# Kernel tuning notes

Measured on AMD Instinct MI355X. Metric: run time of the kernel, lower is better.

## Reference

```python
import jax, jax.numpy as jnp
import numpy as np

N = 6000
E = 48000
NODE_TYPE_SIZE = 9
OBSTACLE = 1
RADIUS = 0.03
EPS = 1e-8


def _safe_norm(x):
    # L2 norm over last dim, safe gradient at 0 (diagonal / self edges)
    sq = jnp.sum(x * x, axis=-1, keepdims=True)
    return jnp.where(sq > 0, jnp.sqrt(jnp.where(sq > 0, sq, 1.0)), 0.0)


def setup_inputs() -> dict:
    key = jax.random.key(0)
    ks = jax.random.split(key, 12)
    world_pos = jax.random.uniform(ks[0], (N, 3), dtype=jnp.float32)
    prev_world_pos = world_pos + 0.001 * jax.random.normal(ks[1], (N, 3), dtype=jnp.float32)
    mesh_pos = jax.random.uniform(ks[2], (N, 2), dtype=jnp.float32)
    node_type = jax.random.randint(ks[3], (N, 1), 0, NODE_TYPE_SIZE)
    senders = jax.random.randint(ks[4], (E,), 0, N)
    receivers = jax.random.randint(ks[5], (E,), 0, N)
    node_mean = jax.random.normal(ks[6], (3 + NODE_TYPE_SIZE,), dtype=jnp.float32)
    node_std = 0.5 + jax.random.uniform(ks[7], (3 + NODE_TYPE_SIZE,), dtype=jnp.float32)
    mesh_mean = jax.random.normal(ks[8], (7,), dtype=jnp.float32)
    mesh_std = 0.5 + jax.random.uniform(ks[9], (7,), dtype=jnp.float32)
    world_mean = jax.random.normal(ks[10], (4,), dtype=jnp.float32)
    world_std = 0.5 + jax.random.uniform(ks[11], (4,), dtype=jnp.float32)
    return dict(world_pos=world_pos, prev_world_pos=prev_world_pos, mesh_pos=mesh_pos,
                node_type=node_type, senders=senders, receivers=receivers,
                node_mean=node_mean, node_std=node_std, mesh_mean=mesh_mean,
                mesh_std=mesh_std, world_mean=world_mean, world_std=world_std)


def reference(world_pos, prev_world_pos, mesh_pos, node_type, senders, receivers,
              node_mean, node_std, mesh_mean, mesh_std, world_mean, world_std):
    n = world_pos.shape[0]
    # --- node features: velocity + one-hot node type, normalized ---
    velocity = world_pos - prev_world_pos
    one_hot = jax.nn.one_hot(node_type[:, 0], NODE_TYPE_SIZE, dtype=world_pos.dtype)
    node_feat = jnp.concatenate([velocity, one_hot], axis=-1)  # [N, 12]
    node_out = (node_feat - node_mean) / jnp.maximum(node_std, EPS)
    # --- radius graph: dense squared-distance matrix + threshold (cdist < r) ---
    sq = jnp.sum(world_pos * world_pos, axis=-1)
    d2 = sq[:, None] + sq[None, :] - 2.0 * (world_pos @ world_pos.T)  # [N, N]
    conn = d2 < RADIUS ** 2
    conn = conn & ~jnp.eye(n, dtype=bool)              # fill_diagonal_(False)
    conn = conn.at[senders, receivers].set(False)      # drop existing mesh edges
    obstacle = node_type[:, 0] == OBSTACLE
    conn = conn & ~obstacle[None, :]                   # no edges into obstacle nodes
    # --- world edge features (dense, masked by connectivity) ---
    rel_world = world_pos[None, :, :] - world_pos[:, None, :]  # [i,j] = pos[j]-pos[i]
    world_feat = jnp.concatenate([rel_world, _safe_norm(rel_world)], axis=-1)  # [N, N, 4]
    world_out = (world_feat - world_mean) / jnp.maximum(world_std, EPS)
    world_out = jnp.where(conn[:, :, None], world_out, 0.0)
    # --- mesh edge features: gather on edge list, normalize ---
    rw = world_pos[senders] - world_pos[receivers]     # [E, 3]
    rm = mesh_pos[senders] - mesh_pos[receivers]       # [E, 2]
    mesh_feat = jnp.concatenate([rw, _safe_norm(rw), rm, _safe_norm(rm)], axis=-1)  # [E, 7]
    mesh_out = (mesh_feat - mesh_mean) / jnp.maximum(mesh_std, EPS)
    # --- unsorted_segment_operation: scatter_add mesh edge features to receivers ---
    agg = jax.ops.segment_sum(mesh_out, receivers, num_segments=n)  # [N, 7]
    return node_out, mesh_out, world_out, agg
```

## Files before the change

kernel.cpp:

```cpp
#include <hip/hip_runtime.h>

#define N_NODES 6000
#define N_EDGES 48000
#define NODE_TYPE_SIZE 9
#define OBSTACLE 1
#define RADIUS2 0.0009f
#define EPS_F 1e-8f

#define OFF_NODE  0
#define OFF_MESH  72000
#define OFF_WORLD 408000
#define OFF_AGG   144408000

#define AUX_NODE_END 72000
#define AUX_AGG_END  (72000 + 42000)
#define AUX_TBL_END  (72000 + 42000 + 6000)

#define TI 128

__global__ void k_aux(const float* __restrict__ wp, const float* __restrict__ pwp,
                      const int* __restrict__ nt, const float* __restrict__ nmean,
                      const float* __restrict__ nstd, float* __restrict__ node_out,
                      float* __restrict__ agg, float4* __restrict__ tbl) {
    int t = blockIdx.x * blockDim.x + threadIdx.x;
    if (t < AUX_NODE_END) {
        int n = t / 12;
        int f = t - n * 12;
        float feat;
        if (f < 3) feat = wp[n * 3 + f] - pwp[n * 3 + f];
        else       feat = (nt[n] == f - 3) ? 1.0f : 0.0f;
        node_out[t] = (feat - nmean[f]) / fmaxf(nstd[f], EPS_F);
    } else if (t < AUX_AGG_END) {
        agg[t - AUX_NODE_END] = 0.0f;
    } else if (t < AUX_TBL_END) {
        int j = t - AUX_AGG_END;
        float x = wp[3 * j + 0], y = wp[3 * j + 1], z = wp[3 * j + 2];
        float sq = x * x + y * y + z * z;
        if (nt[j] == OBSTACLE) sq = 1e30f;
        tbl[j] = make_float4(x, y, z, sq);
    }
}

__global__ void k_mesh(const float* __restrict__ wp, const float* __restrict__ mp,
                       const int* __restrict__ senders, const int* __restrict__ receivers,
                       const float* __restrict__ mean, const float* __restrict__ stdv,
                       float* __restrict__ mesh_out, float* __restrict__ agg) {
    int e = blockIdx.x * blockDim.x + threadIdx.x;
    if (e >= N_EDGES) return;
    int s = senders[e];
    int r = receivers[e];
    float rwx = wp[3 * s + 0] - wp[3 * r + 0];
    float rwy = wp[3 * s + 1] - wp[3 * r + 1];
    float rwz = wp[3 * s + 2] - wp[3 * r + 2];
    float nrw = sqrtf(rwx * rwx + rwy * rwy + rwz * rwz);
    float rmx = mp[2 * s + 0] - mp[2 * r + 0];
    float rmy = mp[2 * s + 1] - mp[2 * r + 1];
    float nrm = sqrtf(rmx * rmx + rmy * rmy);
    float feats[7] = {rwx, rwy, rwz, nrw, rmx, rmy, nrm};
    #pragma unroll
    for (int k = 0; k < 7; ++k) {
        float o = (feats[k] - mean[k]) / fmaxf(stdv[k], EPS_F);
        mesh_out[e * 7 + k] = o;
        atomicAdd(&agg[r * 7 + k], o);
    }
}

__global__ void k_pairs(const float4* __restrict__ tbl, const float* __restrict__ mean,
                        const float* __restrict__ stdv, float4* __restrict__ world_out) {
    __shared__ float4 si[TI];
    const int i0 = blockIdx.y * TI;
    const int ni = (N_NODES - i0 < TI) ? (N_NODES - i0) : TI;
    if (threadIdx.x < ni) si[threadIdx.x] = tbl[i0 + threadIdx.x];
    __syncthreads();

    const int j = blockIdx.x * 256 + threadIdx.x;
    if (j >= N_NODES) return;
    const float4 pj = tbl[j];
    if (pj.w > 1e29f) return;

    const float m0 = mean[0], m1 = mean[1], m2 = mean[2], m3 = mean[3];
    const float s0 = fmaxf(stdv[0], EPS_F), s1 = fmaxf(stdv[1], EPS_F);
    const float s2 = fmaxf(stdv[2], EPS_F), s3 = fmaxf(stdv[3], EPS_F);

    for (int k = 0; k < ni; ++k) {
        float4 pi = si[k];
        float sqi = pi.x * pi.x + pi.y * pi.y + pi.z * pi.z;
        float dot = pi.x * pj.x + pi.y * pj.y + pi.z * pj.z;
        float d2 = sqi + pj.w - 2.0f * dot;
        int i = i0 + k;
        if (d2 < RADIUS2 && i != j) {
            float rx = pj.x - pi.x, ry = pj.y - pi.y, rz = pj.z - pi.z;
            float nrm = sqrtf(rx * rx + ry * ry + rz * rz);
            float4 v;
            v.x = (rx  - m0) / s0;
            v.y = (ry  - m1) / s1;
            v.z = (rz  - m2) / s2;
            v.w = (nrm - m3) / s3;
            world_out[(size_t)i * N_NODES + j] = v;
        }
    }
}

__global__ void k_edge_zero(const int* __restrict__ senders, const int* __restrict__ receivers,
                            float4* __restrict__ world_out) {
    int e = blockIdx.x * blockDim.x + threadIdx.x;
    if (e >= N_EDGES) return;
    world_out[(size_t)senders[e] * N_NODES + receivers[e]] = make_float4(0.0f, 0.0f, 0.0f, 0.0f);
}

extern "C" void kernel_launch(void* const* d_in, const int* in_sizes, int n_in,
                              void* d_out, int out_size, void* d_ws, size_t ws_size,
                              hipStream_t stream) {
    const float* wp    = (const float*)d_in[0];
    const float* pwp   = (const float*)d_in[1];
    const float* mp    = (const float*)d_in[2];
    const int*   nt    = (const int*)d_in[3];
    const int*   snd   = (const int*)d_in[4];
    const int*   rcv   = (const int*)d_in[5];
    const float* nmean = (const float*)d_in[6];
    const float* nstd  = (const float*)d_in[7];
    const float* mmean = (const float*)d_in[8];
    const float* mstd  = (const float*)d_in[9];
    const float* wmean = (const float*)d_in[10];
    const float* wstd  = (const float*)d_in[11];

    float* out       = (float*)d_out;
    float* node_out  = out + OFF_NODE;
    float* mesh_out  = out + OFF_MESH;
    float* world_out = out + OFF_WORLD;
    float* agg       = out + OFF_AGG;
    float4* tbl      = (float4*)d_ws;

    k_aux<<<(AUX_TBL_END + 255) / 256, 256, 0, stream>>>(
        wp, pwp, nt, nmean, nstd, node_out, agg, tbl);

    k_mesh<<<(N_EDGES + 255) / 256, 256, 0, stream>>>(
        wp, mp, snd, rcv, mmean, mstd, mesh_out, agg);

    hipMemsetAsync(world_out, 0, (size_t)N_NODES * N_NODES * 4 * sizeof(float), stream);

    dim3 pgrid((N_NODES + 255) / 256, (N_NODES + TI - 1) / TI);
    k_pairs<<<pgrid, 256, 0, stream>>>(tbl, wmean, wstd, (float4*)world_out);

    k_edge_zero<<<(N_EDGES + 255) / 256, 256, 0, stream>>>(snd, rcv, (float4*)world_out);
}
```

Baseline: 168.7 us.

## Fuse world_out zero-fill into pair kernel, writing every element once

Drops the separate hipMemsetAsync of the 576 MB dense world_out buffer. The pair kernel now uses one block row per node i and writes either the normalized feature or zero for every (i,j). The goal is to avoid touching the large output twice (memset, then scattered sparse writes). In exchange it gives up the shared-memory tiling of i and recomputes the per-pair distance test with a one-row-per-block grid (24x6000 blocks).

```diff
diff --git a/kernel.cpp b/kernel.cpp
--- a/kernel.cpp
+++ b/kernel.cpp
@@ -15,8 +15,6 @@
 #define AUX_NODE_END 72000
 #define AUX_AGG_END  (72000 + 42000)
 #define AUX_TBL_END  (72000 + 42000 + 6000)
-
-#define TI 128
 
 __global__ void k_aux(const float* __restrict__ wp, const float* __restrict__ pwp,
                       const int* __restrict__ nt, const float* __restrict__ nmean,
@@ -65,40 +63,26 @@
     }
 }
 
-__global__ void k_pairs(const float4* __restrict__ tbl, const float* __restrict__ mean,
+__global__ void k_world(const float4* __restrict__ tbl, const float* __restrict__ mean,
                         const float* __restrict__ stdv, float4* __restrict__ world_out) {
-    __shared__ float4 si[TI];
-    const int i0 = blockIdx.y * TI;
-    const int ni = (N_NODES - i0 < TI) ? (N_NODES - i0) : TI;
-    if (threadIdx.x < ni) si[threadIdx.x] = tbl[i0 + threadIdx.x];
-    __syncthreads();
-
+    const int i = blockIdx.y;
     const int j = blockIdx.x * 256 + threadIdx.x;
     if (j >= N_NODES) return;
+    const float4 pi = tbl[i];
     const float4 pj = tbl[j];
-    if (pj.w > 1e29f) return;
-
-    const float m0 = mean[0], m1 = mean[1], m2 = mean[2], m3 = mean[3];
-    const float s0 = fmaxf(stdv[0], EPS_F), s1 = fmaxf(stdv[1], EPS_F);
-    const float s2 = fmaxf(stdv[2], EPS_F), s3 = fmaxf(stdv[3], EPS_F);
-
-    for (int k = 0; k < ni; ++k) {
-        float4 pi = si[k];
-        float sqi = pi.x * pi.x + pi.y * pi.y + pi.z * pi.z;
-        float dot = pi.x * pj.x + pi.y * pj.y + pi.z * pj.z;
-        float d2 = sqi + pj.w - 2.0f * dot;
-        int i = i0 + k;
-        if (d2 < RADIUS2 && i != j) {
-            float rx = pj.x - pi.x, ry = pj.y - pi.y, rz = pj.z - pi.z;
-            float nrm = sqrtf(rx * rx + ry * ry + rz * rz);
-            float4 v;
-            v.x = (rx  - m0) / s0;
-            v.y = (ry  - m1) / s1;
-            v.z = (rz  - m2) / s2;
-            v.w = (nrm - m3) / s3;
-            world_out[(size_t)i * N_NODES + j] = v;
-        }
+    const float sqi = pi.x * pi.x + pi.y * pi.y + pi.z * pi.z;
+    const float dot = pi.x * pj.x + pi.y * pj.y + pi.z * pj.z;
+    const float d2 = sqi + pj.w - 2.0f * dot;
+    float4 v = make_float4(0.0f, 0.0f, 0.0f, 0.0f);
+    if (d2 < RADIUS2 && i != j) {
+        float rx = pj.x - pi.x, ry = pj.y - pi.y, rz = pj.z - pi.z;
+        float nrm = sqrtf(rx * rx + ry * ry + rz * rz);
+        v.x = (rx  - mean[0]) / fmaxf(stdv[0], EPS_F);
+        v.y = (ry  - mean[1]) / fmaxf(stdv[1], EPS_F);
+        v.z = (rz  - mean[2]) / fmaxf(stdv[2], EPS_F);
+        v.w = (nrm - mean[3]) / fmaxf(stdv[3], EPS_F);
     }
+    world_out[(size_t)i * N_NODES + j] = v;
 }
 
 __global__ void k_edge_zero(const int* __restrict__ senders, const int* __restrict__ receivers,
@@ -137,10 +121,8 @@
     k_mesh<<<(N_EDGES + 255) / 256, 256, 0, stream>>>(
         wp, mp, snd, rcv, mmean, mstd, mesh_out, agg);
 
-    hipMemsetAsync(world_out, 0, (size_t)N_NODES * N_NODES * 4 * sizeof(float), stream);
-
-    dim3 pgrid((N_NODES + 255) / 256, (N_NODES + TI - 1) / TI);
-    k_pairs<<<pgrid, 256, 0, stream>>>(tbl, wmean, wstd, (float4*)world_out);
+    dim3 wgrid((N_NODES + 255) / 256, N_NODES);
+    k_world<<<wgrid, 256, 0, stream>>>(tbl, wmean, wstd, (float4*)world_out);
 
     k_edge_zero<<<(N_EDGES + 255) / 256, 256, 0, stream>>>(snd, rcv, (float4*)world_out);
 }
```

After: 147.4 us. 1.14x faster.
